# Kernel optimization log

Hardware: AMD Instinct MI355X
Metric: run time of the kernel (lower is better)

## Reference

```python
import jax, jax.numpy as jnp
import numpy as np
import math

B, S, D, H = 4, 2048, 512, 8
DK = D // H
EPS = 1e-6

def _xavier(key, shape):
    fan_in, fan_out = shape[1], shape[0]
    a = math.sqrt(6.0 / (fan_in + fan_out))
    return jax.random.uniform(key, shape, jnp.float32, -a, a)

def setup_inputs() -> dict:
    key = jax.random.key(0)
    ks = jax.random.split(key, 8)
    return {
        "x_q": jax.random.normal(ks[0], (B, S, D), jnp.float32),
        "x_k": jax.random.normal(ks[1], (B, S, D), jnp.float32),
        "Wq": _xavier(ks[2], (D, D)),
        "Wk": _xavier(ks[3], (D, D)),
        "Wv": _xavier(ks[4], (D, D)),
        "Wg": jnp.zeros((D, D), jnp.float32),      # gating weight init to 0
        "bg": jnp.ones((D,), jnp.float32),          # gating bias init to 1
        "Wo": _xavier(ks[5], (D, D)),
        "bo": jnp.zeros((D,), jnp.float32),
        "gamma": jnp.ones((D,), jnp.float32),
        "beta": jnp.zeros((D,), jnp.float32),
    }

def _ln(x, gamma, beta):
    mu = jnp.mean(x, axis=-1, keepdims=True)
    var = jnp.var(x, axis=-1, keepdims=True)
    return (x - mu) * jax.lax.rsqrt(var + EPS) * gamma + beta

def reference(x_q, x_k, Wq, Wk, Wv, Wg, bg, Wo, bo, gamma, beta):
    xq = _ln(x_q, gamma, beta)          # [B,S,D]
    xk = _ln(x_k, gamma, beta)
    q = xq @ Wq.T                        # nn.Linear: x @ W^T (no bias)
    k = xk @ Wk.T
    v = xk @ Wv.T
    q = q.reshape(B, S, H, DK)
    k = k.reshape(B, S, H, DK)
    v = v.reshape(B, S, H, DK)
    attn = jnp.einsum('bshd,bthd->bhst', q, k) / math.sqrt(DK)  # [B,H,S,S]
    attn = jax.nn.softmax(attn, axis=-1) * jax.nn.softmax(attn, axis=-2)
    out = jnp.einsum('bhst,bthd->bshd', attn, v).reshape(B, S, D)
    gate = jax.nn.sigmoid(xq @ Wg.T + bg)
    return (out * gate) @ Wo.T + bo
```

## Files before the change

kernel.cpp:

```cpp
#include <hip/hip_runtime.h>

#define BB 4
#define SS 2048
#define DD 512
#define HH 8
#define RR (BB * SS)
#define BH (BB * HH)

typedef unsigned short u16;
typedef unsigned int   u32;
typedef __attribute__((ext_vector_type(4))) float f32x4;
typedef __attribute__((ext_vector_type(8))) short bf16x8;

__device__ __forceinline__ float bf2f(u16 u) { return __uint_as_float(((u32)u) << 16); }
__device__ __forceinline__ u16 f2bf(float f) {
    u32 x = __float_as_uint(f);
    return (u16)((x + 0x7fffu + ((x >> 16) & 1u)) >> 16);
}
__device__ __forceinline__ bool is_bf16(const void* gamma) {
    return *(const u32*)gamma == 0x3F803F80u;
}
__device__ __forceinline__ float ldin(const void* p, size_t i, bool b16) {
    return b16 ? bf2f(((const u16*)p)[i]) : ((const float*)p)[i];
}
__device__ __forceinline__ float expc(float x) { return __expf(fminf(x, 60.f)); }
__device__ __forceinline__ float e2sum(float x) {
    return __builtin_amdgcn_exp2f(fminf(x * 1.44269504f, 86.5617f));
}
__device__ __forceinline__ float e2pv(float x) {
    return __builtin_amdgcn_exp2f(fminf(x * 2.88539008f, 86.5617f));
}

__global__ __launch_bounds__(256) void k_ln(
    const void* xq, const void* xk, const void* gamma, const void* beta,
    u16* __restrict__ lnq, u16* __restrict__ lnk, float* l_col)
{
    bool b16 = is_bf16(gamma);
    int row = blockIdx.x, tid = threadIdx.x;
    const void* x = blockIdx.y ? xk : xq;
    u16* o = blockIdx.y ? lnk : lnq;
    size_t base = (size_t)row * DD;

    if (blockIdx.y == 0 && row < 256) l_col[row * 256 + tid] = 0.f;

    float x0 = ldin(x, base + tid * 2, b16);
    float x1 = ldin(x, base + tid * 2 + 1, b16);
    float s = x0 + x1, ss = x0 * x0 + x1 * x1;
    for (int m = 1; m < 64; m <<= 1) { s += __shfl_xor(s, m); ss += __shfl_xor(ss, m); }
    __shared__ float ws4[4], wss4[4], mu_s, rs_s;
    int wv = tid >> 6;
    if ((tid & 63) == 0) { ws4[wv] = s; wss4[wv] = ss; }
    __syncthreads();
    if (tid == 0) {
        float S1 = ws4[0] + ws4[1] + ws4[2] + ws4[3];
        float S2 = wss4[0] + wss4[1] + wss4[2] + wss4[3];
        float mu = S1 / (float)DD;
        float var = S2 / (float)DD - mu * mu;
        mu_s = mu; rs_s = rsqrtf(fmaxf(var, 0.f) + 1e-6f);
    }
    __syncthreads();
    float mu = mu_s, rstd = rs_s;
    float g0 = ldin(gamma, tid * 2, b16), g1 = ldin(gamma, tid * 2 + 1, b16);
    float b0 = ldin(beta, tid * 2, b16),  b1 = ldin(beta, tid * 2 + 1, b16);
    o[base + tid * 2]     = f2bf((x0 - mu) * rstd * g0 + b0);
    o[base + tid * 2 + 1] = f2bf((x1 - mu) * rstd * g1 + b1);
}

__global__ __launch_bounds__(256) void k_proj4(
    const u16* __restrict__ lnq, const u16* __restrict__ lnk,
    const void* Wq, const void* Wk, const void* Wv, const void* Wg,
    const void* bg, const void* gamma,
    u16* __restrict__ qb, u16* __restrict__ kb,
    u16* __restrict__ vT, u16* __restrict__ gb)
{
    __shared__ __align__(16) u16 As[128][64];
    __shared__ __align__(16) u16 Bs[128][64];
    bool b16 = is_bf16(gamma);
    int which = blockIdx.z;
    const u16* A = (which <= 1) ? lnq : lnk;
    const void* W = (which == 0) ? Wq : (which == 1) ? Wg : (which == 2) ? Wk : Wv;
    u16* C = (which == 0) ? qb : (which == 1) ? gb : (which == 2) ? kb : vT;

    int tid = threadIdx.x;
    int lane = tid & 63, wave = tid >> 6;
    int r = lane & 15, q4 = lane >> 4;
    int m0 = blockIdx.y * 128, n0 = blockIdx.x * 128;
    int moff = (wave >> 1) * 64, noff = (wave & 1) * 64;
    const int K = DD, N = DD;

    f32x4 acc[4][4];
    for (int i = 0; i < 4; ++i)
        for (int j = 0; j < 4; ++j) acc[i][j] = (f32x4){0.f, 0.f, 0.f, 0.f};

    for (int k0 = 0; k0 < K; k0 += 64) {
        #pragma unroll
        for (int t = 0; t < 4; ++t) {
            int e = t * 2048 + tid * 8;
            int row = e >> 6, kk = e & 63;
            int ksw = kk ^ ((row & 7) * 8);
            *(uint4*)&As[row][ksw] = *(const uint4*)&A[(size_t)(m0 + row) * K + k0 + kk];
            if (b16) {
                *(uint4*)&Bs[row][ksw] =
                    *(const uint4*)&((const u16*)W)[(size_t)(n0 + row) * K + k0 + kk];
            } else {
                const float* wp = (const float*)W + (size_t)(n0 + row) * K + k0 + kk;
                float4 w0 = *(const float4*)wp;
                float4 w1 = *(const float4*)(wp + 4);
                ushort4 lo, hi;
                lo.x = f2bf(w0.x); lo.y = f2bf(w0.y); lo.z = f2bf(w0.z); lo.w = f2bf(w0.w);
                hi.x = f2bf(w1.x); hi.y = f2bf(w1.y); hi.z = f2bf(w1.z); hi.w = f2bf(w1.w);
                *(ushort4*)&Bs[row][ksw] = lo;
                *(ushort4*)&Bs[row][ksw + 4] = hi;
            }
        }
        __syncthreads();
        #pragma unroll
        for (int ksp = 0; ksp < 2; ++ksp) {
            int kb2 = ksp * 32 + q4 * 8;
            bf16x8 af[4], bfr[4];
            #pragma unroll
            for (int i = 0; i < 4; ++i) {
                int rowm = moff + i * 16 + r;
                af[i] = *(const bf16x8*)&As[rowm][kb2 ^ ((rowm & 7) * 8)];
                int rown = noff + i * 16 + r;
                bfr[i] = *(const bf16x8*)&Bs[rown][kb2 ^ ((rown & 7) * 8)];
            }
            #pragma unroll
            for (int i = 0; i < 4; ++i)
                #pragma unroll
                for (int j = 0; j < 4; ++j)
                    acc[i][j] = __builtin_amdgcn_mfma_f32_16x16x32_bf16(af[i], bfr[j], acc[i][j], 0, 0, 0);
        }
        __syncthreads();
    }

    if (which == 3) {
        int b = m0 >> 11;
        int sb = (m0 & 2047) + moff + q4 * 4;
        #pragma unroll
        for (int j = 0; j < 4; ++j) {
            int n = n0 + noff + j * 16 + r;
            int h = n >> 6, dkl = n & 63;
            size_t vbase = (((size_t)b * 8 + h) * 64 + dkl) * SS;
            #pragma unroll
            for (int i = 0; i < 4; ++i) {
                ushort4 wv;
                wv.x = f2bf(acc[i][j][0]); wv.y = f2bf(acc[i][j][1]);
                wv.z = f2bf(acc[i][j][2]); wv.w = f2bf(acc[i][j][3]);
                *(ushort4*)&C[vbase + sb + i * 16] = wv;
            }
        }
    } else {
        #pragma unroll
        for (int j = 0; j < 4; ++j) {
            int col = n0 + noff + j * 16 + r;
            float bj = (which == 1) ? ldin(bg, col, b16) : 0.f;
            #pragma unroll
            for (int i = 0; i < 4; ++i) {
                int rowb = m0 + moff + i * 16 + q4 * 4;
                #pragma unroll
                for (int g = 0; g < 4; ++g) {
                    float v = acc[i][j][g];
                    if (which == 1) v = 1.f / (1.f + expc(-(v + bj)));
                    else if (which == 0) v *= 0.125f;
                    C[(size_t)(rowb + g) * N + col] = f2bf(v);
                }
            }
        }
    }
}

__global__ __launch_bounds__(256) void k_sum(
    const u16* __restrict__ qm, const u16* __restrict__ km,
    float* __restrict__ l_row, float* __restrict__ l_col)
{
    __shared__ __align__(16) u16 Qs[128][64];
    __shared__ __align__(16) u16 Ks[128][64];
    __shared__ float colS[SS];
    int tid = threadIdx.x, lane = tid & 63, wave = tid >> 6;
    int r = lane & 15, q4 = lane >> 4;
    int s0 = blockIdx.x * 128;
    int bh = blockIdx.y, b = bh >> 3, h = bh & 7;
    size_t hb = (size_t)b * SS * DD + (size_t)h * 64;

    #pragma unroll
    for (int t = 0; t < 4; ++t) {
        int e = t * 2048 + tid * 8;
        int row = e >> 6, kk = e & 63;
        *(uint4*)&Qs[row][kk ^ ((row & 7) * 8)] = *(const uint4*)&qm[hb + (size_t)(s0 + row) * DD + kk];
    }
    for (int i = tid; i < SS; i += 256) colS[i] = 0.f;
    __syncthreads();

    int moff = wave * 32;
    bf16x8 aq[2][2];
    #pragma unroll
    for (int m = 0; m < 2; ++m)
        #pragma unroll
        for (int ksp = 0; ksp < 2; ++ksp) {
            int rowm = moff + m * 16 + r;
            aq[m][ksp] = *(const bf16x8*)&Qs[rowm][(ksp * 32 + q4 * 8) ^ ((rowm & 7) * 8)];
        }

    float rs[2][4] = {};
    for (int t0 = 0; t0 < SS; t0 += 128) {
        #pragma unroll
        for (int t = 0; t < 4; ++t) {
            int e = t * 2048 + tid * 8;
            int row = e >> 6, kk = e & 63;
            *(uint4*)&Ks[row][kk ^ ((row & 7) * 8)] = *(const uint4*)&km[hb + (size_t)(t0 + row) * DD + kk];
        }
        __syncthreads();

        f32x4 acc[2][8];
        #pragma unroll
        for (int m = 0; m < 2; ++m)
            #pragma unroll
            for (int j = 0; j < 8; ++j) acc[m][j] = (f32x4){0.f, 0.f, 0.f, 0.f};
        #pragma unroll
        for (int ksp = 0; ksp < 2; ++ksp) {
            int kb2 = ksp * 32 + q4 * 8;
            bf16x8 bk[8];
            #pragma unroll
            for (int j = 0; j < 8; ++j) {
                int n = j * 16 + r;
                bk[j] = *(const bf16x8*)&Ks[n][kb2 ^ ((n & 7) * 8)];
            }
            #pragma unroll
            for (int m = 0; m < 2; ++m)
                #pragma unroll
                for (int j = 0; j < 8; ++j)
                    acc[m][j] = __builtin_amdgcn_mfma_f32_16x16x32_bf16(aq[m][ksp], bk[j], acc[m][j], 0, 0, 0);
        }

        #pragma unroll
        for (int j = 0; j < 8; ++j) {
            float cj = 0.f;
            #pragma unroll
            for (int m = 0; m < 2; ++m) {
                float e0 = e2sum(acc[m][j][0]);
                float e1 = e2sum(acc[m][j][1]);
                float e2 = e2sum(acc[m][j][2]);
                float e3 = e2sum(acc[m][j][3]);
                rs[m][0] += e0; rs[m][1] += e1; rs[m][2] += e2; rs[m][3] += e3;
                cj += (e0 + e1) + (e2 + e3);
            }
            cj += __shfl_xor(cj, 16); cj += __shfl_xor(cj, 32);
            if (q4 == 0) atomicAdd(&colS[t0 + j * 16 + r], cj);
        }
        __syncthreads();
    }
    #pragma unroll
    for (int m = 0; m < 2; ++m)
        #pragma unroll
        for (int g = 0; g < 4; ++g) {
            float v = rs[m][g];
            v += __shfl_xor(v, 1); v += __shfl_xor(v, 2);
            v += __shfl_xor(v, 4); v += __shfl_xor(v, 8);
            if (r == 0) l_row[(size_t)bh * SS + s0 + moff + m * 16 + q4 * 4 + g] = v;
        }
    for (int i = tid; i < SS; i += 256)
        atomicAdd(&l_col[(size_t)bh * SS + i], colS[i]);
}

__global__ void k_rcp(const float* __restrict__ l_row, float* __restrict__ inv_r, int n)
{
    int i = blockIdx.x * blockDim.x + threadIdx.x;
    if (i < n) inv_r[i] = 1.f / fmaxf(l_row[i], 1e-30f);
}

__global__ __launch_bounds__(256) void k_vscale(
    u16* __restrict__ vT, const float* __restrict__ l_col)
{
    int row = blockIdx.x;
    int bh = row >> 6;
    int t = threadIdx.x * 8;
    size_t base = (size_t)row * SS + t;
    const float* lc = &l_col[(size_t)bh * SS + t];
    bf16x8 v = *(const bf16x8*)&vT[base];
    float4 c0 = *(const float4*)lc;
    float4 c1 = *(const float4*)(lc + 4);
    float s[8] = {1.f / fmaxf(c0.x, 1e-30f), 1.f / fmaxf(c0.y, 1e-30f),
                  1.f / fmaxf(c0.z, 1e-30f), 1.f / fmaxf(c0.w, 1e-30f),
                  1.f / fmaxf(c1.x, 1e-30f), 1.f / fmaxf(c1.y, 1e-30f),
                  1.f / fmaxf(c1.z, 1e-30f), 1.f / fmaxf(c1.w, 1e-30f)};
    bf16x8 o;
    #pragma unroll
    for (int e = 0; e < 8; ++e)
        o[e] = (short)f2bf(bf2f((u16)v[e]) * s[e]);
    *(bf16x8*)&vT[base] = o;
}

__global__ __launch_bounds__(256) void k_pv(
    const u16* __restrict__ qm, const u16* __restrict__ km, const u16* __restrict__ vT,
    const float* __restrict__ inv_r,
    const u16* __restrict__ gate, u16* __restrict__ og)
{
    __shared__ __align__(16) u16 Ep[64][128];
    __shared__ __align__(16) u16 KV[8192];
    int tid = threadIdx.x, lane = tid & 63, wave = tid >> 6;
    int r = lane & 15, q4 = lane >> 4;
    int s0 = blockIdx.x * 64;
    int bh = blockIdx.y, b = bh >> 3, h = bh & 7;
    size_t hb = (size_t)b * SS * DD + (size_t)h * 64;
    int moff = wave * 16;

    #pragma unroll
    for (int t = 0; t < 2; ++t) {
        int e = t * 2048 + tid * 8;
        int row = e >> 6, kk = e & 63;
        *(uint4*)&Ep[row][kk ^ ((row & 7) * 8)] = *(const uint4*)&qm[hb + (size_t)(s0 + row) * DD + kk];
    }
    __syncthreads();
    bf16x8 aq[2];
    #pragma unroll
    for (int ksp = 0; ksp < 2; ++ksp) {
        int rowm = moff + r;
        aq[ksp] = *(const bf16x8*)&Ep[rowm][(ksp * 32 + q4 * 8) ^ ((rowm & 7) * 8)];
    }
    __syncthreads();

    f32x4 acco[4];
    for (int j = 0; j < 4; ++j) acco[j] = (f32x4){0.f, 0.f, 0.f, 0.f};

    int sl = moff + r, swz = (sl & 7) * 8;

    for (int t0 = 0; t0 < SS; t0 += 128) {
        #pragma unroll
        for (int t = 0; t < 4; ++t) {
            int e = t * 2048 + tid * 8;
            int row = e >> 6, kk = e & 63;
            *(uint4*)&KV[row * 64 + (kk ^ ((row & 7) * 8))] =
                *(const uint4*)&km[hb + (size_t)(t0 + row) * DD + kk];
        }
        __syncthreads();

        f32x4 accs[8];
        #pragma unroll
        for (int m = 0; m < 8; ++m) accs[m] = (f32x4){0.f, 0.f, 0.f, 0.f};
        #pragma unroll
        for (int ksp = 0; ksp < 2; ++ksp) {
            int kb2 = ksp * 32 + q4 * 8;
            bf16x8 ak[8];
            #pragma unroll
            for (int m = 0; m < 8; ++m) {
                int n = m * 16 + r;
                ak[m] = *(const bf16x8*)&KV[n * 64 + (kb2 ^ ((n & 7) * 8))];
            }
            #pragma unroll
            for (int m = 0; m < 8; ++m)
                accs[m] = __builtin_amdgcn_mfma_f32_16x16x32_bf16(ak[m], aq[ksp], accs[m], 0, 0, 0);
        }
        __syncthreads();

        #pragma unroll
        for (int c = 0; c < 4; ++c) {
            int e = c * 256 + tid;
            int row = e >> 4, tc = (e & 15) * 8;
            *(uint4*)&KV[row * 128 + (tc ^ ((row & 7) * 8))] =
                *(const uint4*)&vT[((size_t)bh * 64 + row) * SS + t0 + tc];
        }
        #pragma unroll
        for (int m = 0; m < 8; ++m) {
            float p0 = e2pv(accs[m][0]);
            float p1 = e2pv(accs[m][1]);
            float p2 = e2pv(accs[m][2]);
            float p3 = e2pv(accs[m][3]);
            u32 w0, w1;
            asm("v_cvt_pk_bf16_f32 %0, %1, %2" : "=v"(w0) : "v"(p0), "v"(p1));
            asm("v_cvt_pk_bf16_f32 %0, %1, %2" : "=v"(w1) : "v"(p2), "v"(p3));
            uint2 pr; pr.x = w0; pr.y = w1;
            *(uint2*)&Ep[sl][(m * 16 + q4 * 4) ^ swz] = pr;
        }
        __syncthreads();

        #pragma unroll
        for (int ksp = 0; ksp < 4; ++ksp) {
            int kb2 = ksp * 32 + q4 * 8;
            bf16x8 ap = *(const bf16x8*)&Ep[sl][kb2 ^ swz];
            bf16x8 bv[4];
            #pragma unroll
            for (int j = 0; j < 4; ++j) {
                int n = j * 16 + r;
                bv[j] = *(const bf16x8*)&KV[n * 128 + (kb2 ^ ((n & 7) * 8))];
            }
            #pragma unroll
            for (int j = 0; j < 4; ++j)
                acco[j] = __builtin_amdgcn_mfma_f32_16x16x32_bf16(ap, bv[j], acco[j], 0, 0, 0);
        }
        __syncthreads();
    }

    #pragma unroll
    for (int g = 0; g < 4; ++g) {
        int srow = s0 + moff + q4 * 4 + g;
        float ir = inv_r[(size_t)bh * SS + srow];
        size_t ob = (size_t)b * SS * DD + (size_t)srow * DD + (size_t)h * 64;
        #pragma unroll
        for (int j = 0; j < 4; ++j) {
            int dk = j * 16 + r;
            og[ob + dk] = f2bf(acco[j][g] * ir * bf2f(gate[ob + dk]));
        }
    }
}

__global__ __launch_bounds__(256) void k_gemm_out(
    const u16* __restrict__ A, const void* W, const void* gamma,
    float* __restrict__ Cf, const void* bias)
{
    __shared__ __align__(16) u16 As[128][64];
    __shared__ __align__(16) u16 Bs[128][64];
    bool b16 = is_bf16(gamma);
    int tid = threadIdx.x;
    int lane = tid & 63, wave = tid >> 6;
    int r = lane & 15, q4 = lane >> 4;
    int m0 = blockIdx.y * 128, n0 = blockIdx.x * 128;
    int moff = (wave >> 1) * 64, noff = (wave & 1) * 64;
    const int K = DD, N = DD;

    f32x4 acc[4][4];
    for (int i = 0; i < 4; ++i)
        for (int j = 0; j < 4; ++j) acc[i][j] = (f32x4){0.f, 0.f, 0.f, 0.f};

    for (int k0 = 0; k0 < K; k0 += 64) {
        #pragma unroll
        for (int t = 0; t < 4; ++t) {
            int e = t * 2048 + tid * 8;
            int row = e >> 6, kk = e & 63;
            int ksw = kk ^ ((row & 7) * 8);
            *(uint4*)&As[row][ksw] = *(const uint4*)&A[(size_t)(m0 + row) * K + k0 + kk];
            if (b16) {
                *(uint4*)&Bs[row][ksw] =
                    *(const uint4*)&((const u16*)W)[(size_t)(n0 + row) * K + k0 + kk];
            } else {
                const float* wp = (const float*)W + (size_t)(n0 + row) * K + k0 + kk;
                float4 w0 = *(const float4*)wp;
                float4 w1 = *(const float4*)(wp + 4);
                ushort4 lo, hi;
                lo.x = f2bf(w0.x); lo.y = f2bf(w0.y); lo.z = f2bf(w0.z); lo.w = f2bf(w0.w);
                hi.x = f2bf(w1.x); hi.y = f2bf(w1.y); hi.z = f2bf(w1.z); hi.w = f2bf(w1.w);
                *(ushort4*)&Bs[row][ksw] = lo;
                *(ushort4*)&Bs[row][ksw + 4] = hi;
            }
        }
        __syncthreads();
        #pragma unroll
        for (int ksp = 0; ksp < 2; ++ksp) {
            int kb2 = ksp * 32 + q4 * 8;
            bf16x8 af[4], bfr[4];
            #pragma unroll
            for (int i = 0; i < 4; ++i) {
                int rowm = moff + i * 16 + r;
                af[i] = *(const bf16x8*)&As[rowm][kb2 ^ ((rowm & 7) * 8)];
                int rown = noff + i * 16 + r;
                bfr[i] = *(const bf16x8*)&Bs[rown][kb2 ^ ((rown & 7) * 8)];
            }
            #pragma unroll
            for (int i = 0; i < 4; ++i)
                #pragma unroll
                for (int j = 0; j < 4; ++j)
                    acc[i][j] = __builtin_amdgcn_mfma_f32_16x16x32_bf16(af[i], bfr[j], acc[i][j], 0, 0, 0);
        }
        __syncthreads();
    }
    #pragma unroll
    for (int j = 0; j < 4; ++j) {
        int col = n0 + noff + j * 16 + r;
        float bj = ldin(bias, col, b16);
        #pragma unroll
        for (int i = 0; i < 4; ++i) {
            int rowb = m0 + moff + i * 16 + q4 * 4;
            #pragma unroll
            for (int g = 0; g < 4; ++g) {
                float v = acc[i][j][g] + bj;
                size_t idx = (size_t)(rowb + g) * N + col;
                if (b16) ((u16*)Cf)[idx] = f2bf(v);
                else     Cf[idx] = v;
            }
        }
    }
}

extern "C" void kernel_launch(void* const* d_in, const int* in_sizes, int n_in,
                              void* d_out, int out_size, void* d_ws, size_t ws_size,
                              hipStream_t stream)
{
    const void* x_q   = d_in[0];
    const void* x_k   = d_in[1];
    const void* Wq    = d_in[2];
    const void* Wk    = d_in[3];
    const void* Wv    = d_in[4];
    const void* Wg    = d_in[5];
    const void* bg    = d_in[6];
    const void* Wo    = d_in[7];
    const void* bo    = d_in[8];
    const void* gamma = d_in[9];
    const void* beta  = d_in[10];

    char* base = (char*)d_ws;
    u16* lnq = (u16*)(base);
    u16* lnk = (u16*)(base + (size_t) 8 * 1024 * 1024);
    u16* qb  = (u16*)(base + (size_t)16 * 1024 * 1024);
    u16* kb  = (u16*)(base + (size_t)24 * 1024 * 1024);
    u16* gb  = (u16*)(base + (size_t)32 * 1024 * 1024);
    float* l_row = (float*)(base + (size_t)40 * 1024 * 1024);
    float* l_col = (float*)(base + (size_t)40 * 1024 * 1024 + 262144);
    float* inv_r = (float*)(base + (size_t)40 * 1024 * 1024 + 524288);
    u16* vT = (u16*)d_out;
    u16* og = lnk;

    k_ln<<<dim3(RR, 2), 256, 0, stream>>>(x_q, x_k, gamma, beta, lnq, lnk, l_col);

    k_proj4<<<dim3(4, 64, 4), 256, 0, stream>>>(lnq, lnk, Wq, Wk, Wv, Wg, bg, gamma,
                                                qb, kb, vT, gb);

    k_sum<<<dim3(SS / 128, BH), 256, 0, stream>>>(qb, kb, l_row, l_col);
    k_rcp<<<dim3(BH * SS / 256), 256, 0, stream>>>(l_row, inv_r, BH * SS);
    k_vscale<<<dim3(BH * 64), 256, 0, stream>>>(vT, l_col);
    k_pv<<<dim3(SS / 64, BH), 256, 0, stream>>>(qb, kb, vT, inv_r, gb, og);

    k_gemm_out<<<dim3(4, 64), 256, 0, stream>>>(og, Wo, gamma, (float*)d_out, bo);
}
```

Baseline: 320.9 us.

## Double k_pv query tile to 128 rows and interleave QK/PV per wave

The PV kernel now processes 128 query rows per block, with each wave owning 32 rows, so every K and V tile loaded from global memory is reused by twice as many queries. K and V tiles are loaded into separate shared buffers together, which removes two of the four barriers per tile iteration. Score computation, exponentiation and the PV MFMA run per 32-column chunk inside each wave, relying on each wave reading only its own rows of Ep. In exchange the grid has half as many blocks, shared memory rises to about 64KB and register pressure grows, which may lower occupancy.

```diff
diff --git a/kernel.cpp b/kernel.cpp
--- a/kernel.cpp
+++ b/kernel.cpp
@@ -296,112 +296,131 @@
     const float* __restrict__ inv_r,
     const u16* __restrict__ gate, u16* __restrict__ og)
 {
-    __shared__ __align__(16) u16 Ep[64][128];
-    __shared__ __align__(16) u16 KV[8192];
+    __shared__ __align__(16) u16 Ep[128][128];
+    __shared__ __align__(16) u16 Kt[128][64];
+    __shared__ __align__(16) u16 Vt[64][128];
     int tid = threadIdx.x, lane = tid & 63, wave = tid >> 6;
     int r = lane & 15, q4 = lane >> 4;
-    int s0 = blockIdx.x * 64;
+    int s0 = blockIdx.x * 128;
     int bh = blockIdx.y, b = bh >> 3, h = bh & 7;
     size_t hb = (size_t)b * SS * DD + (size_t)h * 64;
-    int moff = wave * 16;
-
-    #pragma unroll
-    for (int t = 0; t < 2; ++t) {
+    size_t vb = (size_t)bh * 64 * SS;
+    int moff = wave * 32;
+    int swz = (r & 7) * 8;
+
+    #pragma unroll
+    for (int t = 0; t < 4; ++t) {
         int e = t * 2048 + tid * 8;
         int row = e >> 6, kk = e & 63;
         *(uint4*)&Ep[row][kk ^ ((row & 7) * 8)] = *(const uint4*)&qm[hb + (size_t)(s0 + row) * DD + kk];
     }
     __syncthreads();
-    bf16x8 aq[2];
-    #pragma unroll
-    for (int ksp = 0; ksp < 2; ++ksp) {
-        int rowm = moff + r;
-        aq[ksp] = *(const bf16x8*)&Ep[rowm][(ksp * 32 + q4 * 8) ^ ((rowm & 7) * 8)];
-    }
+    bf16x8 aq[2][2];
+    #pragma unroll
+    for (int ms = 0; ms < 2; ++ms)
+        #pragma unroll
+        for (int kq = 0; kq < 2; ++kq) {
+            int rowm = moff + ms * 16 + r;
+            aq[ms][kq] = *(const bf16x8*)&Ep[rowm][(kq * 32 + q4 * 8) ^ ((rowm & 7) * 8)];
+        }
     __syncthreads();
 
-    f32x4 acco[4];
-    for (int j = 0; j < 4; ++j) acco[j] = (f32x4){0.f, 0.f, 0.f, 0.f};
-
-    int sl = moff + r, swz = (sl & 7) * 8;
+    f32x4 acco[2][4];
+    #pragma unroll
+    for (int ms = 0; ms < 2; ++ms)
+        #pragma unroll
+        for (int j = 0; j < 4; ++j) acco[ms][j] = (f32x4){0.f, 0.f, 0.f, 0.f};
 
     for (int t0 = 0; t0 < SS; t0 += 128) {
         #pragma unroll
         for (int t = 0; t < 4; ++t) {
             int e = t * 2048 + tid * 8;
             int row = e >> 6, kk = e & 63;
-            *(uint4*)&KV[row * 64 + (kk ^ ((row & 7) * 8))] =
+            *(uint4*)&Kt[row][kk ^ ((row & 7) * 8)] =
                 *(const uint4*)&km[hb + (size_t)(t0 + row) * DD + kk];
         }
-        __syncthreads();
-
-        f32x4 accs[8];
-        #pragma unroll
-        for (int m = 0; m < 8; ++m) accs[m] = (f32x4){0.f, 0.f, 0.f, 0.f};
-        #pragma unroll
-        for (int ksp = 0; ksp < 2; ++ksp) {
-            int kb2 = ksp * 32 + q4 * 8;
-            bf16x8 ak[8];
-            #pragma unroll
-            for (int m = 0; m < 8; ++m) {
-                int n = m * 16 + r;
-                ak[m] = *(const bf16x8*)&KV[n * 64 + (kb2 ^ ((n & 7) * 8))];
-            }
-            #pragma unroll
-            for (int m = 0; m < 8; ++m)
-                accs[m] = __builtin_amdgcn_mfma_f32_16x16x32_bf16(ak[m], aq[ksp], accs[m], 0, 0, 0);
-        }
-        __syncthreads();
-
         #pragma unroll
         for (int c = 0; c < 4; ++c) {
             int e = c * 256 + tid;
             int row = e >> 4, tc = (e & 15) * 8;
-            *(uint4*)&KV[row * 128 + (tc ^ ((row & 7) * 8))] =
-                *(const uint4*)&vT[((size_t)bh * 64 + row) * SS + t0 + tc];
-        }
-        #pragma unroll
-        for (int m = 0; m < 8; ++m) {
-            float p0 = e2pv(accs[m][0]);
-            float p1 = e2pv(accs[m][1]);
-            float p2 = e2pv(accs[m][2]);
-            float p3 = e2pv(accs[m][3]);
-            u32 w0, w1;
-            asm("v_cvt_pk_bf16_f32 %0, %1, %2" : "=v"(w0) : "v"(p0), "v"(p1));
-            asm("v_cvt_pk_bf16_f32 %0, %1, %2" : "=v"(w1) : "v"(p2), "v"(p3));
-            uint2 pr; pr.x = w0; pr.y = w1;
-            *(uint2*)&Ep[sl][(m * 16 + q4 * 4) ^ swz] = pr;
-        }
-        __syncthreads();
-
-        #pragma unroll
-        for (int ksp = 0; ksp < 4; ++ksp) {
-            int kb2 = ksp * 32 + q4 * 8;
-            bf16x8 ap = *(const bf16x8*)&Ep[sl][kb2 ^ swz];
-            bf16x8 bv[4];
+            *(uint4*)&Vt[row][tc ^ ((row & 7) * 8)] =
+                *(const uint4*)&vT[vb + (size_t)row * SS + t0 + tc];
+        }
+        __syncthreads();
+
+        #pragma unroll
+        for (int mp = 0; mp < 4; ++mp) {
+            f32x4 accs[2][2];
+            #pragma unroll
+            for (int ms = 0; ms < 2; ++ms)
+                #pragma unroll
+                for (int mi = 0; mi < 2; ++mi) accs[ms][mi] = (f32x4){0.f, 0.f, 0.f, 0.f};
+            #pragma unroll
+            for (int kq = 0; kq < 2; ++kq) {
+                int kb2 = kq * 32 + q4 * 8;
+                bf16x8 ak[2];
+                #pragma unroll
+                for (int mi = 0; mi < 2; ++mi) {
+                    int n = (mp * 2 + mi) * 16 + r;
+                    ak[mi] = *(const bf16x8*)&Kt[n][kb2 ^ ((n & 7) * 8)];
+                }
+                #pragma unroll
+                for (int ms = 0; ms < 2; ++ms)
+                    #pragma unroll
+                    for (int mi = 0; mi < 2; ++mi)
+                        accs[ms][mi] = __builtin_amdgcn_mfma_f32_16x16x32_bf16(ak[mi], aq[ms][kq], accs[ms][mi], 0, 0, 0);
+            }
+            #pragma unroll
+            for (int ms = 0; ms < 2; ++ms) {
+                int sl = moff + ms * 16 + r;
+                #pragma unroll
+                for (int mi = 0; mi < 2; ++mi) {
+                    int m = mp * 2 + mi;
+                    float p0 = e2pv(accs[ms][mi][0]);
+                    float p1 = e2pv(accs[ms][mi][1]);
+                    float p2 = e2pv(accs[ms][mi][2]);
+                    float p3 = e2pv(accs[ms][mi][3]);
+                    u32 w0, w1;
+                    asm("v_cvt_pk_bf16_f32 %0, %1, %2" : "=v"(w0) : "v"(p0), "v"(p1));
+                    asm("v_cvt_pk_bf16_f32 %0, %1, %2" : "=v"(w1) : "v"(p2), "v"(p3));
+                    uint2 pr; pr.x = w0; pr.y = w1;
+                    *(uint2*)&Ep[sl][(m * 16 + q4 * 4) ^ swz] = pr;
+                }
+            }
+            asm volatile("" ::: "memory");
+            {
+                int kb2 = mp * 32 + q4 * 8;
+                bf16x8 ap0 = *(const bf16x8*)&Ep[moff + r][kb2 ^ swz];
+                bf16x8 ap1 = *(const bf16x8*)&Ep[moff + 16 + r][kb2 ^ swz];
+                bf16x8 bv[4];
+                #pragma unroll
+                for (int j = 0; j < 4; ++j) {
+                    int n = j * 16 + r;
+                    bv[j] = *(const bf16x8*)&Vt[n][kb2 ^ ((n & 7) * 8)];
+                }
+                #pragma unroll
+                for (int j = 0; j < 4; ++j) {
+                    acco[0][j] = __builtin_amdgcn_mfma_f32_16x16x32_bf16(ap0, bv[j], acco[0][j], 0, 0, 0);
+                    acco[1][j] = __builtin_amdgcn_mfma_f32_16x16x32_bf16(ap1, bv[j], acco[1][j], 0, 0, 0);
+                }
+            }
+        }
+        __syncthreads();
+    }
+
+    #pragma unroll
+    for (int ms = 0; ms < 2; ++ms)
+        #pragma unroll
+        for (int g = 0; g < 4; ++g) {
+            int srow = s0 + moff + ms * 16 + q4 * 4 + g;
+            float ir = inv_r[(size_t)bh * SS + srow];
+            size_t ob = (size_t)b * SS * DD + (size_t)srow * DD + (size_t)h * 64;
             #pragma unroll
             for (int j = 0; j < 4; ++j) {
-                int n = j * 16 + r;
-                bv[j] = *(const bf16x8*)&KV[n * 128 + (kb2 ^ ((n & 7) * 8))];
-            }
-            #pragma unroll
-            for (int j = 0; j < 4; ++j)
-                acco[j] = __builtin_amdgcn_mfma_f32_16x16x32_bf16(ap, bv[j], acco[j], 0, 0, 0);
-        }
-        __syncthreads();
-    }
-
-    #pragma unroll
-    for (int g = 0; g < 4; ++g) {
-        int srow = s0 + moff + q4 * 4 + g;
-        float ir = inv_r[(size_t)bh * SS + srow];
-        size_t ob = (size_t)b * SS * DD + (size_t)srow * DD + (size_t)h * 64;
-        #pragma unroll
-        for (int j = 0; j < 4; ++j) {
-            int dk = j * 16 + r;
-            og[ob + dk] = f2bf(acco[j][g] * ir * bf2f(gate[ob + dk]));
-        }
-    }
+                int dk = j * 16 + r;
+                og[ob + dk] = f2bf(acco[ms][j][g] * ir * bf2f(gate[ob + dk]));
+            }
+        }
 }
 
 __global__ __launch_bounds__(256) void k_gemm_out(
@@ -517,7 +536,7 @@
     k_sum<<<dim3(SS / 128, BH), 256, 0, stream>>>(qb, kb, l_row, l_col);
     k_rcp<<<dim3(BH * SS / 256), 256, 0, stream>>>(l_row, inv_r, BH * SS);
     k_vscale<<<dim3(BH * 64), 256, 0, stream>>>(vT, l_col);
-    k_pv<<<dim3(SS / 64, BH), 256, 0, stream>>>(qb, kb, vT, inv_r, gb, og);
+    k_pv<<<dim3(SS / 128, BH), 256, 0, stream>>>(qb, kb, vT, inv_r, gb, og);
 
     k_gemm_out<<<dim3(4, 64), 256, 0, stream>>>(og, Wo, gamma, (float*)d_out, bo);
 }
```

After: 306.7 us. 4.4% less time.
